# Kernel optimization log

Measured on AMD Instinct MI355X. Metric: run time of the kernel, lower is better.

The kernel has to match this reference:

```python
import jax, jax.numpy as jnp
import numpy as np


def setup_inputs() -> dict:
    key = jax.random.key(0)
    k1, k2, k3, k4, k5 = jax.random.split(key, 5)
    B, H, W, F = 32, 32, 32, 768
    x = jax.random.normal(k1, (B, H, W, F), dtype=jnp.float32)
    fc_w = jax.random.normal(k2, (2, F), dtype=jnp.float32) * 0.02
    fc_b = jax.random.normal(k3, (2,), dtype=jnp.float32) * 0.02
    fc_final_w = jax.random.normal(k4, (2, F), dtype=jnp.float32) * 0.02
    fc_final_b = jax.random.normal(k5, (2,), dtype=jnp.float32) * 0.02
    return {"x": x, "fc_w": fc_w, "fc_b": fc_b,
            "fc_final_w": fc_final_w, "fc_final_b": fc_final_b}


def reference(x, fc_w, fc_b, fc_final_w, fc_final_b):
    B = x.shape[0]
    F = x.shape[-1]
    tokens = x.reshape(B, -1, F)                              # [B, T, F]
    norm = jnp.linalg.norm(tokens, axis=-1, keepdims=True)
    nt = tokens / norm                                        # unit-norm tokens
    # full T x T cosine-similarity attention (faithful to original einsum)
    attention = jnp.einsum('btf,bTf->btT', nt, nt)            # [B, T, T]
    attention = jax.nn.softmax(attention, axis=-1)
    # per-token cancer probability via small linear head
    logits = jnp.einsum('btf,cf->btc', tokens, fc_w) + fc_b   # [B, T, 2]
    cancer_probs = jax.nn.softmax(logits, axis=-1)[:, :, 1]   # [B, T]
    idx = jnp.argmax(cancer_probs, axis=1)                    # [B]
    # gather the single attention row selected by argmax
    attention_idx = jnp.take_along_axis(attention, idx[:, None, None], axis=1)[:, 0, :]  # [B, T]
    attention_idx = attention_idx * cancer_probs
    attention_idx = attention_idx / attention_idx.sum(axis=-1, keepdims=True)
    x_fused = jnp.einsum('bt,btf->bf', attention_idx, tokens)  # [B, F]
    return jnp.einsum('bf,cf->bc', x_fused, fc_final_w) + fc_final_b
```

## Files before the change

### kernel.cpp

```cpp
#include <hip/hip_runtime.h>
#include <hip/hip_bf16.h>
#include <math.h>

#define BATCH 32
#define T 1024
#define F 768


__global__ __launch_bounds__(256) void k1_token_stats(
    const float* __restrict__ x, const float* __restrict__ fc_w,
    const float* __restrict__ fc_b, const float* __restrict__ fc_final_w,
    float4* __restrict__ stats, unsigned long long* __restrict__ best)
{
    const int wave = threadIdx.x >> 6;
    const int lane = threadIdx.x & 63;
    const int b     = blockIdx.x >> 5;
    const int tbase = (blockIdx.x & 31) * 32;

    float4 wd[3], f0[3], f1[3];
    #pragma unroll
    for (int j = 0; j < 3; ++j) {
        const int off = j * 256 + lane * 4;
        float4 a = *(const float4*)(fc_w + off);
        float4 c = *(const float4*)(fc_w + F + off);
        wd[j] = make_float4(a.x - c.x, a.y - c.y, a.z - c.z, a.w - c.w);
        f0[j] = *(const float4*)(fc_final_w + off);
        f1[j] = *(const float4*)(fc_final_w + F + off);
    }
    const float bias01 = fc_b[0] - fc_b[1];

    float bp = -1.f; int bidx = 0;
    #pragma unroll
    for (int it = 0; it < 8; ++it) {
        const int t = tbase + it * 4 + wave;
        const float* tok = x + ((size_t)b * T + t) * F;
        float asq = 0.f, da = 0.f, af0 = 0.f, af1 = 0.f;
        #pragma unroll
        for (int j = 0; j < 3; ++j) {
            float4 v = *(const float4*)(tok + j * 256 + lane * 4);
            asq += v.x*v.x     + v.y*v.y     + v.z*v.z     + v.w*v.w;
            da  += v.x*wd[j].x + v.y*wd[j].y + v.z*wd[j].z + v.w*wd[j].w;
            af0 += v.x*f0[j].x + v.y*f0[j].y + v.z*f0[j].z + v.w*f0[j].w;
            af1 += v.x*f1[j].x + v.y*f1[j].y + v.z*f1[j].z + v.w*f1[j].w;
        }
        #pragma unroll
        for (int d = 32; d > 0; d >>= 1) {
            asq += __shfl_xor(asq, d);
            da  += __shfl_xor(da,  d);
            af0 += __shfl_xor(af0, d);
            af1 += __shfl_xor(af1, d);
        }
        const float p = 1.f / (1.f + expf(da + bias01));
        if (lane == 0)
            stats[(size_t)b * T + t] = make_float4(p, af0, af1, 1.f / sqrtf(asq));
        if (p > bp) { bp = p; bidx = t; }
    }

    __shared__ float sp[4]; __shared__ int si[4];
    if (lane == 0) { sp[wave] = bp; si[wave] = bidx; }
    __syncthreads();
    if (threadIdx.x == 0) {
        float P = sp[0]; int I = si[0];
        for (int w = 1; w < 4; ++w)
            if (sp[w] > P || (sp[w] == P && si[w] < I)) { P = sp[w]; I = si[w]; }
        best[blockIdx.x] =
            ((unsigned long long)__float_as_uint(P) << 32) |
            (unsigned long long)(0xFFFFFFFFu - (unsigned)I);
    }
}

__global__ __launch_bounds__(256) void k3_attn_row(
    const float* __restrict__ x, const float4* __restrict__ stats,
    const unsigned long long* __restrict__ best, float4* __restrict__ part)
{
    const int b     = blockIdx.x >> 6;
    const int tbase = (blockIdx.x & 63) * 16;
    const int wave = threadIdx.x >> 6;
    const int lane = threadIdx.x & 63;

    unsigned long long pk = (lane < 32) ? best[b * 32 + lane] : 0ull;
    #pragma unroll
    for (int d = 32; d > 0; d >>= 1) {
        const unsigned long long o = __shfl_xor(pk, d);
        pk = o > pk ? o : pk;
    }
    const int idx = (int)(0xFFFFFFFFu - (unsigned)(pk & 0xFFFFFFFFull));

    const float4 qs = stats[(size_t)b * T + idx];
    const float* qg = x + ((size_t)b * T + idx) * F;
    float4 q[3];
    #pragma unroll
    for (int j = 0; j < 3; ++j) {
        float4 v = *(const float4*)(qg + j * 256 + lane * 4);
        q[j] = make_float4(v.x * qs.w, v.y * qs.w, v.z * qs.w, v.w * qs.w);
    }

    float den = 0.f, n0 = 0.f, n1 = 0.f;
    #pragma unroll
    for (int it = 0; it < 4; ++it) {
        const int t = tbase + it * 4 + wave;
        const float* tok = x + ((size_t)b * T + t) * F;
        const float4 st = stats[(size_t)b * T + t];
        float acc = 0.f;
        #pragma unroll
        for (int j = 0; j < 3; ++j) {
            float4 v = *(const float4*)(tok + j * 256 + lane * 4);
            acc += v.x*q[j].x + v.y*q[j].y + v.z*q[j].z + v.w*q[j].w;
        }
        #pragma unroll
        for (int d = 32; d > 0; d >>= 1) acc += __shfl_xor(acc, d);
        const float w = expf(acc * st.w) * st.x;
        den += w; n0 += w * st.y; n1 += w * st.z;
    }

    __shared__ float red[4][3];
    if (lane == 0) { red[wave][0] = den; red[wave][1] = n0; red[wave][2] = n1; }
    __syncthreads();
    if (threadIdx.x == 0) {
        float D = 0.f, N0 = 0.f, N1 = 0.f;
        for (int w = 0; w < 4; ++w) { D += red[w][0]; N0 += red[w][1]; N1 += red[w][2]; }
        part[(size_t)b * 64 + (blockIdx.x & 63)] = make_float4(D, N0, N1, 0.f);
    }
}

__global__ __launch_bounds__(64) void k4_finalize(
    const float4* __restrict__ part, const float* __restrict__ fc_final_b,
    float* __restrict__ out)
{
    const int b = blockIdx.x;
    const int lane = threadIdx.x;
    float4 v = part[(size_t)b * 64 + lane];
    float D = v.x, N0 = v.y, N1 = v.z;
    #pragma unroll
    for (int d = 32; d > 0; d >>= 1) {
        D  += __shfl_xor(D,  d);
        N0 += __shfl_xor(N0, d);
        N1 += __shfl_xor(N1, d);
    }
    if (lane == 0) {
        out[b * 2 + 0] = N0 / D + fc_final_b[0];
        out[b * 2 + 1] = N1 / D + fc_final_b[1];
    }
}

extern "C" void kernel_launch(void* const* d_in, const int* in_sizes, int n_in,
                              void* d_out, int out_size, void* d_ws, size_t ws_size,
                              hipStream_t stream) {
    const float* x          = (const float*)d_in[0];
    const float* fc_w       = (const float*)d_in[1];
    const float* fc_b       = (const float*)d_in[2];
    const float* fc_final_w = (const float*)d_in[3];
    const float* fc_final_b = (const float*)d_in[4];
    float* out = (float*)d_out;

    char* ws = (char*)d_ws;
    unsigned long long* best = (unsigned long long*)ws;
    float4* part  = (float4*)(ws + 8192);
    float4* stats = (float4*)(ws + 65536);

    k1_token_stats<<<dim3(BATCH * 32), 256, 0, stream>>>(
        x, fc_w, fc_b, fc_final_w, stats, best);
    k3_attn_row<<<dim3(BATCH * 64), 256, 0, stream>>>(x, stats, best, part);
    k4_finalize<<<dim3(BATCH), 64, 0, stream>>>(part, fc_final_b, out);
}
```

Measured before the change: 171.7 us.

## Fuse three kernels into cooperative kernel with grid sync and prefetch rows

Merges the token-stats, attention-row and finalize kernels into one cooperative kernel, separated by grid-wide barriers, with the old three-launch path kept as a fallback. Each block reuses the same batch and token range in both phases, so phase B can find the rows it just read still in L2. Both phases also software-prefetch the next token row into registers. Phase B is regridded to 1024 blocks of 32 tokens. The aim is to remove launch gaps and increase L2 reuse, at the cost of grid-sync overhead, higher register pressure and the requirement that all 1024 blocks be co-resident.

```diff
diff --git a/kernel.cpp b/kernel.cpp
--- a/kernel.cpp
+++ b/kernel.cpp
@@ -1,21 +1,28 @@
 #include <hip/hip_runtime.h>
-#include <hip/hip_bf16.h>
+#include <hip/hip_cooperative_groups.h>
 #include <math.h>
+
+namespace cg = cooperative_groups;
 
 #define BATCH 32
 #define T 1024
 #define F 768
 
 
-__global__ __launch_bounds__(256) void k1_token_stats(
+__device__ __forceinline__ void load_row(const float* __restrict__ p, int lane, float4 v[3]) {
+    #pragma unroll
+    for (int j = 0; j < 3; ++j) v[j] = *(const float4*)(p + j * 256 + lane * 4);
+}
+
+__device__ __forceinline__ void phaseA(
     const float* __restrict__ x, const float* __restrict__ fc_w,
     const float* __restrict__ fc_b, const float* __restrict__ fc_final_w,
-    float4* __restrict__ stats, unsigned long long* __restrict__ best)
+    float4* __restrict__ stats, unsigned long long* __restrict__ best, int blk)
 {
     const int wave = threadIdx.x >> 6;
     const int lane = threadIdx.x & 63;
-    const int b     = blockIdx.x >> 5;
-    const int tbase = (blockIdx.x & 31) * 32;
+    const int b     = blk >> 5;
+    const int tbase = (blk & 31) * 32;
 
     float4 wd[3], f0[3], f1[3];
     #pragma unroll
@@ -30,30 +37,37 @@
     const float bias01 = fc_b[0] - fc_b[1];
 
     float bp = -1.f; int bidx = 0;
+    float4 v[3], nxt[3];
+    load_row(x + ((size_t)b * T + tbase + wave) * F, lane, v);
     #pragma unroll
     for (int it = 0; it < 8; ++it) {
         const int t = tbase + it * 4 + wave;
-        const float* tok = x + ((size_t)b * T + t) * F;
-        float asq = 0.f, da = 0.f, af0 = 0.f, af1 = 0.f;
+        if (it < 7)
+            load_row(x + ((size_t)b * T + t + 4) * F, lane, nxt);
+        float asq = 0.f, da = 0.f, a0 = 0.f, a1 = 0.f;
         #pragma unroll
         for (int j = 0; j < 3; ++j) {
-            float4 v = *(const float4*)(tok + j * 256 + lane * 4);
-            asq += v.x*v.x     + v.y*v.y     + v.z*v.z     + v.w*v.w;
-            da  += v.x*wd[j].x + v.y*wd[j].y + v.z*wd[j].z + v.w*wd[j].w;
-            af0 += v.x*f0[j].x + v.y*f0[j].y + v.z*f0[j].z + v.w*f0[j].w;
-            af1 += v.x*f1[j].x + v.y*f1[j].y + v.z*f1[j].z + v.w*f1[j].w;
+            float4 w = v[j];
+            asq += w.x*w.x     + w.y*w.y     + w.z*w.z     + w.w*w.w;
+            da  += w.x*wd[j].x + w.y*wd[j].y + w.z*wd[j].z + w.w*wd[j].w;
+            a0  += w.x*f0[j].x + w.y*f0[j].y + w.z*f0[j].z + w.w*f0[j].w;
+            a1  += w.x*f1[j].x + w.y*f1[j].y + w.z*f1[j].z + w.w*f1[j].w;
         }
         #pragma unroll
         for (int d = 32; d > 0; d >>= 1) {
             asq += __shfl_xor(asq, d);
             da  += __shfl_xor(da,  d);
-            af0 += __shfl_xor(af0, d);
-            af1 += __shfl_xor(af1, d);
+            a0  += __shfl_xor(a0,  d);
+            a1  += __shfl_xor(a1,  d);
         }
         const float p = 1.f / (1.f + expf(da + bias01));
         if (lane == 0)
-            stats[(size_t)b * T + t] = make_float4(p, af0, af1, 1.f / sqrtf(asq));
+            stats[(size_t)b * T + t] = make_float4(p, a0, a1, 1.f / sqrtf(asq));
         if (p > bp) { bp = p; bidx = t; }
+        if (it < 7) {
+            #pragma unroll
+            for (int j = 0; j < 3; ++j) v[j] = nxt[j];
+        }
     }
 
     __shared__ float sp[4]; __shared__ int si[4];
@@ -63,20 +77,19 @@
         float P = sp[0]; int I = si[0];
         for (int w = 1; w < 4; ++w)
             if (sp[w] > P || (sp[w] == P && si[w] < I)) { P = sp[w]; I = si[w]; }
-        best[blockIdx.x] =
-            ((unsigned long long)__float_as_uint(P) << 32) |
-            (unsigned long long)(0xFFFFFFFFu - (unsigned)I);
-    }
-}
-
-__global__ __launch_bounds__(256) void k3_attn_row(
+        best[blk] = ((unsigned long long)__float_as_uint(P) << 32) |
+                    (unsigned long long)(0xFFFFFFFFu - (unsigned)I);
+    }
+}
+
+__device__ __forceinline__ void phaseB(
     const float* __restrict__ x, const float4* __restrict__ stats,
-    const unsigned long long* __restrict__ best, float4* __restrict__ part)
-{
-    const int b     = blockIdx.x >> 6;
-    const int tbase = (blockIdx.x & 63) * 16;
+    const unsigned long long* __restrict__ best, float4* __restrict__ part, int blk)
+{
     const int wave = threadIdx.x >> 6;
     const int lane = threadIdx.x & 63;
+    const int b     = blk >> 5;
+    const int tbase = (blk & 31) * 32;
 
     unsigned long long pk = (lane < 32) ? best[b * 32 + lane] : 0ull;
     #pragma unroll
@@ -87,30 +100,34 @@
     const int idx = (int)(0xFFFFFFFFu - (unsigned)(pk & 0xFFFFFFFFull));
 
     const float4 qs = stats[(size_t)b * T + idx];
-    const float* qg = x + ((size_t)b * T + idx) * F;
     float4 q[3];
+    load_row(x + ((size_t)b * T + idx) * F, lane, q);
     #pragma unroll
     for (int j = 0; j < 3; ++j) {
-        float4 v = *(const float4*)(qg + j * 256 + lane * 4);
-        q[j] = make_float4(v.x * qs.w, v.y * qs.w, v.z * qs.w, v.w * qs.w);
+        q[j].x *= qs.w; q[j].y *= qs.w; q[j].z *= qs.w; q[j].w *= qs.w;
     }
 
     float den = 0.f, n0 = 0.f, n1 = 0.f;
-    #pragma unroll
-    for (int it = 0; it < 4; ++it) {
+    float4 v[3], nxt[3];
+    load_row(x + ((size_t)b * T + tbase + wave) * F, lane, v);
+    #pragma unroll
+    for (int it = 0; it < 8; ++it) {
         const int t = tbase + it * 4 + wave;
-        const float* tok = x + ((size_t)b * T + t) * F;
+        if (it < 7)
+            load_row(x + ((size_t)b * T + t + 4) * F, lane, nxt);
         const float4 st = stats[(size_t)b * T + t];
         float acc = 0.f;
         #pragma unroll
-        for (int j = 0; j < 3; ++j) {
-            float4 v = *(const float4*)(tok + j * 256 + lane * 4);
-            acc += v.x*q[j].x + v.y*q[j].y + v.z*q[j].z + v.w*q[j].w;
-        }
+        for (int j = 0; j < 3; ++j)
+            acc += v[j].x*q[j].x + v[j].y*q[j].y + v[j].z*q[j].z + v[j].w*q[j].w;
         #pragma unroll
         for (int d = 32; d > 0; d >>= 1) acc += __shfl_xor(acc, d);
         const float w = expf(acc * st.w) * st.x;
         den += w; n0 += w * st.y; n1 += w * st.z;
+        if (it < 7) {
+            #pragma unroll
+            for (int j = 0; j < 3; ++j) v[j] = nxt[j];
+        }
     }
 
     __shared__ float red[4][3];
@@ -119,17 +136,16 @@
     if (threadIdx.x == 0) {
         float D = 0.f, N0 = 0.f, N1 = 0.f;
         for (int w = 0; w < 4; ++w) { D += red[w][0]; N0 += red[w][1]; N1 += red[w][2]; }
-        part[(size_t)b * 64 + (blockIdx.x & 63)] = make_float4(D, N0, N1, 0.f);
-    }
-}
-
-__global__ __launch_bounds__(64) void k4_finalize(
+        part[blk] = make_float4(D, N0, N1, 0.f);
+    }
+}
+
+__device__ __forceinline__ void phaseC(
     const float4* __restrict__ part, const float* __restrict__ fc_final_b,
-    float* __restrict__ out)
-{
-    const int b = blockIdx.x;
-    const int lane = threadIdx.x;
-    float4 v = part[(size_t)b * 64 + lane];
+    float* __restrict__ out, int b)
+{
+    const int lane = threadIdx.x & 63;
+    float4 v = (lane < 32) ? part[b * 32 + lane] : make_float4(0.f, 0.f, 0.f, 0.f);
     float D = v.x, N0 = v.y, N1 = v.z;
     #pragma unroll
     for (int d = 32; d > 0; d >>= 1) {
@@ -142,6 +158,38 @@
         out[b * 2 + 1] = N1 / D + fc_final_b[1];
     }
 }
+
+__global__ __launch_bounds__(256, 4) void fused_all(
+    const float* __restrict__ x, const float* __restrict__ fc_w,
+    const float* __restrict__ fc_b, const float* __restrict__ fc_final_w,
+    const float* __restrict__ fc_final_b,
+    float4* __restrict__ stats, unsigned long long* __restrict__ best,
+    float4* __restrict__ part, float* __restrict__ out)
+{
+    cg::grid_group grid = cg::this_grid();
+    phaseA(x, fc_w, fc_b, fc_final_w, stats, best, blockIdx.x);
+    grid.sync();
+    phaseB(x, stats, best, part, blockIdx.x);
+    grid.sync();
+    if (blockIdx.x < BATCH && threadIdx.x < 64)
+        phaseC(part, fc_final_b, out, blockIdx.x);
+}
+
+__global__ __launch_bounds__(256, 4) void k1_token_stats(
+    const float* __restrict__ x, const float* __restrict__ fc_w,
+    const float* __restrict__ fc_b, const float* __restrict__ fc_final_w,
+    float4* __restrict__ stats, unsigned long long* __restrict__ best)
+{ phaseA(x, fc_w, fc_b, fc_final_w, stats, best, blockIdx.x); }
+
+__global__ __launch_bounds__(256, 4) void k3_attn_row(
+    const float* __restrict__ x, const float4* __restrict__ stats,
+    const unsigned long long* __restrict__ best, float4* __restrict__ part)
+{ phaseB(x, stats, best, part, blockIdx.x); }
+
+__global__ __launch_bounds__(64) void k4_finalize(
+    const float4* __restrict__ part, const float* __restrict__ fc_final_b,
+    float* __restrict__ out)
+{ phaseC(part, fc_final_b, out, blockIdx.x); }
 
 extern "C" void kernel_launch(void* const* d_in, const int* in_sizes, int n_in,
                               void* d_out, int out_size, void* d_ws, size_t ws_size,
@@ -158,8 +206,16 @@
     float4* part  = (float4*)(ws + 8192);
     float4* stats = (float4*)(ws + 65536);
 
-    k1_token_stats<<<dim3(BATCH * 32), 256, 0, stream>>>(
-        x, fc_w, fc_b, fc_final_w, stats, best);
-    k3_attn_row<<<dim3(BATCH * 64), 256, 0, stream>>>(x, stats, best, part);
-    k4_finalize<<<dim3(BATCH), 64, 0, stream>>>(part, fc_final_b, out);
-}
+    void* args[] = { (void*)&x, (void*)&fc_w, (void*)&fc_b, (void*)&fc_final_w,
+                     (void*)&fc_final_b, (void*)&stats, (void*)&best,
+                     (void*)&part, (void*)&out };
+    hipError_t e = hipLaunchCooperativeKernel((const void*)fused_all,
+                                              dim3(BATCH * 32), dim3(256),
+                                              args, 0u, stream);
+    if (e != hipSuccess) {
+        k1_token_stats<<<dim3(BATCH * 32), 256, 0, stream>>>(
+            x, fc_w, fc_b, fc_final_w, stats, best);
+        k3_attn_row<<<dim3(BATCH * 32), 256, 0, stream>>>(x, stats, best, part);
+        k4_finalize<<<dim3(BATCH), 64, 0, stream>>>(part, fc_final_b, out);
+    }
+}
```

Result: slower. 396.2 us (+130.7%).
